# Optimization experiments

Measured on AMD Instinct MI355X. Metric: run time of the kernel, lower is better.

## Reference

```python
import jax, jax.numpy as jnp
import numpy as np

B, N, E = 8, 2000, 32000
LAT, STY, NF = 128, 64, 10
HEADS, HID = 4, 128
OUT = 3 + NF  # 13
EPS = 1e-5
SLOPE = 0.2


def _lin(k, fi, fo):
    return jax.random.normal(k, (fi, fo), dtype=jnp.float32) / np.sqrt(fi)


def setup_inputs() -> dict:
    key = jax.random.key(0)
    ks = jax.random.split(key, 32)
    inp = {
        'z': jax.random.normal(ks[0], (B, LAT), dtype=jnp.float32),
        'template_x': jax.random.normal(ks[1], (N, NF), dtype=jnp.float32),
        'template_edge_index': jax.random.randint(ks[2], (2, E), 0, N, dtype=jnp.int32),
        # style MLP
        'mlp_w1': _lin(ks[3], LAT, 256), 'mlp_b1': jnp.zeros((256,), jnp.float32),
        'mlp_w2': _lin(ks[4], 256, 512), 'mlp_b2': jnp.zeros((512,), jnp.float32),
        'mlp_w3': _lin(ks[5], 512, STY), 'mlp_b3': jnp.zeros((STY,), jnp.float32),
        # GAT1: in = NF + STY = 74 -> heads*HID = 512, concat
        'gat1_w': _lin(ks[6], NF + STY, HEADS * HID),
        'gat1_as': jax.random.normal(ks[7], (HEADS, HID), jnp.float32) * 0.1,
        'gat1_ad': jax.random.normal(ks[8], (HEADS, HID), jnp.float32) * 0.1,
        'gat1_b': jnp.zeros((HEADS * HID,), jnp.float32),
        'ln1_g': jnp.ones((HEADS * HID,), jnp.float32), 'ln1_b': jnp.zeros((HEADS * HID,), jnp.float32),
        # GAT2: 512 -> 512, concat
        'gat2_w': _lin(ks[9], HEADS * HID, HEADS * HID),
        'gat2_as': jax.random.normal(ks[10], (HEADS, HID), jnp.float32) * 0.1,
        'gat2_ad': jax.random.normal(ks[11], (HEADS, HID), jnp.float32) * 0.1,
        'gat2_b': jnp.zeros((HEADS * HID,), jnp.float32),
        'ln2_g': jnp.ones((HEADS * HID,), jnp.float32), 'ln2_b': jnp.zeros((HEADS * HID,), jnp.float32),
        # GAT3: 512 -> 13, 1 head, no concat
        'gat3_w': _lin(ks[12], HEADS * HID, OUT),
        'gat3_as': jax.random.normal(ks[13], (1, OUT), jnp.float32) * 0.1,
        'gat3_ad': jax.random.normal(ks[14], (1, OUT), jnp.float32) * 0.1,
        'gat3_b': jnp.zeros((OUT,), jnp.float32),
    }
    return inp


def gat_conv(x, src, dst, n_nodes, W, a_src, a_dst, bias, heads, out_ch, concat):
    # x: [NT, F_in]; per-head linear transform
    h = (x @ W).reshape(-1, heads, out_ch)              # [NT, H, C]
    als = jnp.sum(h * a_src[None], axis=-1)             # [NT, H]
    ald = jnp.sum(h * a_dst[None], axis=-1)             # [NT, H]
    logits = jax.nn.leaky_relu(als[src] + ald[dst], SLOPE)   # [E, H]
    # segment softmax over destination nodes (self-loops guarantee nonempty segments)
    mx = jax.ops.segment_max(logits, dst, num_segments=n_nodes)
    alpha = jnp.exp(logits - mx[dst])
    den = jax.ops.segment_sum(alpha, dst, num_segments=n_nodes)
    alpha = alpha / den[dst]                             # [E, H]
    msgs = h[src] * alpha[:, :, None]                    # [E, H, C]
    out = jax.ops.segment_sum(msgs, dst, num_segments=n_nodes)  # [NT, H, C]
    if concat:
        return out.reshape(n_nodes, heads * out_ch) + bias
    return out.mean(axis=1) + bias


def layer_norm(x, g, b):
    mu = jnp.mean(x, axis=-1, keepdims=True)
    var = jnp.mean((x - mu) ** 2, axis=-1, keepdims=True)
    return (x - mu) * jax.lax.rsqrt(var + EPS) * g + b


def reference(z, template_x, template_edge_index,
              mlp_w1, mlp_b1, mlp_w2, mlp_b2, mlp_w3, mlp_b3,
              gat1_w, gat1_as, gat1_ad, gat1_b, ln1_g, ln1_b,
              gat2_w, gat2_as, gat2_ad, gat2_b, ln2_g, ln2_b,
              gat3_w, gat3_as, gat3_ad, gat3_b):
    bsz = z.shape[0]
    n = template_x.shape[0]
    nt = bsz * n
    # batch the template graph: replicate nodes, offset edge indices per graph
    x = jnp.tile(template_x, (bsz, 1))                                  # [NT, NF]
    off = (jnp.arange(bsz, dtype=template_edge_index.dtype) * n)
    ei = (template_edge_index[:, None, :] + off[None, :, None]).reshape(2, -1)  # [2, B*E]
    loops = jnp.arange(nt, dtype=ei.dtype)
    src = jnp.concatenate([ei[0], loops])
    dst = jnp.concatenate([ei[1], loops])
    # style MLP
    s = jax.nn.leaky_relu(z @ mlp_w1 + mlp_b1, SLOPE)
    s = jax.nn.leaky_relu(s @ mlp_w2 + mlp_b2, SLOPE)
    s = s @ mlp_w3 + mlp_b3                                             # [B, STY]
    s_exp = jnp.repeat(s, n, axis=0)                                    # [NT, STY]
    H0 = jnp.concatenate([x, s_exp], axis=1)
    H1 = jax.nn.leaky_relu(gat_conv(H0, src, dst, nt, gat1_w, gat1_as, gat1_ad, gat1_b, HEADS, HID, True), SLOPE)
    H1n = layer_norm(H1, ln1_g, ln1_b)
    H2 = jax.nn.leaky_relu(gat_conv(H1n, src, dst, nt, gat2_w, gat2_as, gat2_ad, gat2_b, HEADS, HID, True), SLOPE)
    H2 = H2 + H1n
    H2n = layer_norm(H2, ln2_g, ln2_b)
    H_out = gat_conv(H2n, src, dst, nt, gat3_w, gat3_as, gat3_ad, gat3_b, 1, OUT, False)  # [NT, 13]
    delta_p = H_out[:, :3]
    delta_f = H_out[:, 3:]
    p_gen = x[:, :3] + delta_p
    X_gen = jnp.concatenate([p_gen, x[:, 3:] + delta_f[:, 3:]], axis=1)  # X[:, :3] overwritten by p_gen
    EF = p_gen[ei[1]] - p_gen[ei[0]]                                     # edge displacement vectors [B*E, 3]
    return X_gen, p_gen, EF
```

## Files before the change

### kernel.cpp

```cpp
#include <hip/hip_runtime.h>
#include <hip/hip_fp16.h>

constexpr int Bz = 8, Nn = 2000, Ee = 32000, NTOT = 16000;
constexpr int XG_OFF = 0, PG_OFF = 160000, EF_OFF = 208000;
#define SLOPE 0.2f
#define EPSL 1e-5f

typedef __attribute__((ext_vector_type(8))) _Float16 f16x8;
typedef __attribute__((ext_vector_type(4))) float float4v;

__device__ __forceinline__ float lrelu(float x) { return x > 0.f ? x : SLOPE * x; }

__device__ __forceinline__ unsigned short f2h(float x) {
  _Float16 hh = (_Float16)x;
  return *(unsigned short*)&hh;
}

__device__ __forceinline__ float wave_max(float v) {
  for (int o = 32; o; o >>= 1) v = fmaxf(v, __shfl_xor(v, o));
  return v;
}
__device__ __forceinline__ float wave_sum(float v) {
  for (int o = 32; o; o >>= 1) v += __shfl_xor(v, o);
  return v;
}

__global__ void hist_k(const int* __restrict__ tei, int* __restrict__ counts) {
  int j = blockIdx.x * 256 + threadIdx.x;
  if (j < Ee) atomicAdd(&counts[tei[Ee + j]], 1);
}

__global__ void scan_k(const int* __restrict__ counts, int* __restrict__ offs) {
  __shared__ int part[256];
  int t = threadIdx.x;
  int loc[8];
  int s = 0;
  for (int i = 0; i < 8; i++) {
    int idx = t * 8 + i;
    int c = (idx < Nn) ? counts[idx] : 0;
    loc[i] = s; s += c;
  }
  part[t] = s;
  __syncthreads();
  for (int o = 1; o < 256; o <<= 1) {
    int v = (t >= o) ? part[t - o] : 0;
    __syncthreads();
    part[t] += v;
    __syncthreads();
  }
  int excl = (t == 0) ? 0 : part[t - 1];
  for (int i = 0; i < 8; i++) {
    int idx = t * 8 + i;
    if (idx < Nn) offs[idx] = excl + loc[i];
  }
  if (t == 255) offs[Nn] = part[255];
}

__global__ void place_k(const int* __restrict__ tei, const int* __restrict__ offs,
                        int* __restrict__ cursor, int* __restrict__ colb) {
  int j = blockIdx.x * 256 + threadIdx.x;
  if (j < Ee) {
    int d = tei[Ee + j];
    int slot = offs[d] + atomicAdd(&cursor[d], 1);
    colb[slot] = tei[j];
  }
}

template <int K, int ACT>
__global__ __launch_bounds__(256) void lin_k(const float* __restrict__ x, const float* __restrict__ w,
                                             const float* __restrict__ bias, float* __restrict__ y,
                                             int O) {
  int gw = blockIdx.x * 4 + (threadIdx.x >> 6);
  int lane = threadIdx.x & 63;
  int bb = gw / O, o = gw - bb * O;
  float acc = 0.f;
#pragma unroll
  for (int k = lane; k < K; k += 64) acc += x[bb * K + k] * w[k * O + o];
  acc = wave_sum(acc);
  if (lane == 0) {
    if (bias) acc += bias[o];
    y[gw] = ACT ? lrelu(acc) : acc;
  }
}

__global__ __launch_bounds__(256) void w2bf_k(const float* __restrict__ W, unsigned short* __restrict__ Bt) {
  __shared__ float tile[32][33];
  int tx = threadIdx.x & 31, ty = threadIdx.x >> 5;
  int x0 = blockIdx.x * 32;
  int y0 = blockIdx.y * 32;
  for (int r = ty; r < 32; r += 8) tile[r][tx] = W[(y0 + r) * 512 + x0 + tx];
  __syncthreads();
  for (int r = ty; r < 32; r += 8) {
    unsigned short v = f2h(tile[tx][r]);
    size_t off = (size_t)(x0 + r) * 512 + (y0 + tx);
#pragma unroll
    for (int cp = 0; cp < 8; cp++) Bt[cp * 262144 + off] = v;
  }
}

__global__ void w3t_k(const float* __restrict__ W, unsigned short* __restrict__ W3t) {
  for (int idx = threadIdx.x; idx < 8192; idx += 256) {
    int col = idx >> 9, k = idx & 511;
    float v = (col < 13) ? W[k * 13 + col] : 0.f;
    W3t[idx] = f2h(v);
  }
}

__global__ __launch_bounds__(256) void wals_k(const float* __restrict__ g2w,
                                              const float* __restrict__ a_s, const float* __restrict__ a_d,
                                              float* __restrict__ wals, float* __restrict__ wald) {
  int c = blockIdx.x;
  int h = threadIdx.x >> 6, lane = threadIdx.x & 63;
  float sa = 0.f, sd = 0.f;
#pragma unroll
  for (int j = lane; j < 128; j += 64) {
    float wv = g2w[c * 512 + h * 128 + j];
    sa += wv * a_s[h * 128 + j];
    sd += wv * a_d[h * 128 + j];
  }
  sa = wave_sum(sa); sd = wave_sum(sd);
  if (lane == 0) { wals[c * 4 + h] = sa; wald[c * 4 + h] = sd; }
}

__global__ __launch_bounds__(256) void tp16_k(const float* __restrict__ tx, const float* __restrict__ g1w,
                                              const float* __restrict__ a_s, const float* __restrict__ a_d,
                                              unsigned short* __restrict__ tp16, float* __restrict__ tpa,
                                              float* __restrict__ tpd) {
  int nl = blockIdx.x;
  int head = threadIdx.x >> 6, lane = threadIdx.x & 63;
  int c = head * 128 + 2 * lane;
  float t0 = 0.f, t1 = 0.f;
#pragma unroll
  for (int k = 0; k < 10; k++) {
    float xv = tx[nl * 10 + k];
    float2 wv = *(const float2*)&g1w[k * 512 + c];
    t0 += xv * wv.x; t1 += xv * wv.y;
  }
  ushort2 st; st.x = f2h(t0); st.y = f2h(t1);
  *(ushort2*)&tp16[(size_t)nl * 512 + c] = st;
  float2 av = *(const float2*)&a_s[c];
  float2 dv = *(const float2*)&a_d[c];
  float pa = wave_sum(t0 * av.x + t1 * av.y);
  float pd = wave_sum(t0 * dv.x + t1 * dv.y);
  if (lane == 0) { tpa[nl * 4 + head] = pa; tpd[nl * 4 + head] = pd; }
}

__global__ void pba_k(const float* __restrict__ pb, const float* __restrict__ a_s,
                      const float* __restrict__ a_d, float* __restrict__ pba, float* __restrict__ pbd) {
  int b = blockIdx.x >> 2, h = blockIdx.x & 3;
  int lane = threadIdx.x;
  int c = h * 128 + 2 * lane;
  float2 pv = *(const float2*)&pb[b * 512 + c];
  float2 av = *(const float2*)&a_s[c];
  float2 dv = *(const float2*)&a_d[c];
  float pa = wave_sum(pv.x * av.x + pv.y * av.y);
  float pd = wave_sum(pv.x * dv.x + pv.y * dv.y);
  if (lane == 0) { pba[b * 4 + h] = pa; pbd[b * 4 + h] = pd; }
}

__global__ __launch_bounds__(256) void agg1_k(const unsigned short* __restrict__ tp16,
                                              const float* __restrict__ tpa, const float* __restrict__ tpd,
                                              const float* __restrict__ pba, const float* __restrict__ pbd,
                                              const float* __restrict__ pb,
                                              const float* __restrict__ bias,
                                              const float* __restrict__ g, const float* __restrict__ beta,
                                              const float* __restrict__ wals, const float* __restrict__ wald,
                                              unsigned short* __restrict__ out,
                                              float* __restrict__ als2, float* __restrict__ ald2,
                                              const int* __restrict__ offs, const int* __restrict__ colb) {
  int blk = blockIdx.x;
  int b = blk & 7, nl = blk >> 3;
  int n = b * Nn + nl;
  int w = threadIdx.x >> 6, lane = threadIdx.x & 63;
  int rs = offs[nl];
  int nit = offs[nl + 1] - rs + 1;
  float aldn = tpd[nl * 4 + w] + pbd[b * 4 + w];
  float pbsrc = pba[b * 4 + w];

  __shared__ unsigned int alpha_u[4][68];
  __shared__ int sgn[64];
  __shared__ float part[4][512];
  __shared__ float invs[4];
  __shared__ float red[8];
  __shared__ float red2[4][8];
  __shared__ float bcs[2];

  __half2 acc2[4];
#pragma unroll
  for (int j = 0; j < 4; j++) acc2[j] = __float2half2_rn(0.f);

  const unsigned short* hbase = tp16 + lane * 8;
  int hd = lane >> 4;

  if (nit <= 64) {
    int se = nl;
    float logit = -3e38f;
    if (lane < nit) {
      se = (lane < nit - 1) ? colb[rs + lane] : nl;
      logit = lrelu(tpa[se * 4 + w] + pbsrc + aldn);
    }
    if (w == 0) sgn[lane] = se;
    float m = wave_max(logit);
    float raw = (lane < nit) ? __expf(logit - m) : 0.f;
    float den = wave_sum(raw);
    if (lane == 0) invs[w] = 1.f / den;
    __half2 a2 = __float2half2_rn(raw);
    alpha_u[w][lane] = *(unsigned int*)&a2;
    __syncthreads();
    int e = w;
    for (; e + 12 < nit; e += 16) {
      uint4 hv[4];
      unsigned int au[4];
#pragma unroll
      for (int i = 0; i < 4; i++) {
        int ei = e + i * 4;
        au[i] = alpha_u[hd][ei];
        hv[i] = *(const uint4*)(hbase + (size_t)sgn[ei] * 512);
      }
#pragma unroll
      for (int i = 0; i < 4; i++) {
        __half2 a2e = *(__half2*)&au[i];
        acc2[0] = __hfma2(a2e, *(__half2*)&hv[i].x, acc2[0]);
        acc2[1] = __hfma2(a2e, *(__half2*)&hv[i].y, acc2[1]);
        acc2[2] = __hfma2(a2e, *(__half2*)&hv[i].z, acc2[2]);
        acc2[3] = __hfma2(a2e, *(__half2*)&hv[i].w, acc2[3]);
      }
    }
    for (; e < nit; e += 4) {
      unsigned int au = alpha_u[hd][e];
      uint4 hv = *(const uint4*)(hbase + (size_t)sgn[e] * 512);
      __half2 a2e = *(__half2*)&au;
      acc2[0] = __hfma2(a2e, *(__half2*)&hv.x, acc2[0]);
      acc2[1] = __hfma2(a2e, *(__half2*)&hv.y, acc2[1]);
      acc2[2] = __hfma2(a2e, *(__half2*)&hv.z, acc2[2]);
      acc2[3] = __hfma2(a2e, *(__half2*)&hv.w, acc2[3]);
    }
  } else {
    float m = -3e38f;
    for (int i = lane; i < nit; i += 64) {
      int se = (i < nit - 1) ? colb[rs + i] : nl;
      m = fmaxf(m, lrelu(tpa[se * 4 + w] + pbsrc + aldn));
    }
    m = wave_max(m);
    float den = 0.f;
    for (int base = 0; base < nit; base += 64) {
      int cnt = min(64, nit - base);
      int se = nl;
      float raw = 0.f;
      if (lane < cnt) {
        int i = base + lane;
        se = (i < nit - 1) ? colb[rs + i] : nl;
        raw = __expf(lrelu(tpa[se * 4 + w] + pbsrc + aldn) - m);
      }
      if (w == 0) sgn[lane] = se;
      den += raw;
      __half2 a2 = __float2half2_rn(raw);
      alpha_u[w][lane] = *(unsigned int*)&a2;
      __syncthreads();
      for (int e = w; e < cnt; e += 4) {
        unsigned int au = alpha_u[hd][e];
        uint4 hv = *(const uint4*)(hbase + (size_t)sgn[e] * 512);
        __half2 a2e = *(__half2*)&au;
        acc2[0] = __hfma2(a2e, *(__half2*)&hv.x, acc2[0]);
        acc2[1] = __hfma2(a2e, *(__half2*)&hv.y, acc2[1]);
        acc2[2] = __hfma2(a2e, *(__half2*)&hv.z, acc2[2]);
        acc2[3] = __hfma2(a2e, *(__half2*)&hv.w, acc2[3]);
      }
      __syncthreads();
    }
    den = wave_sum(den);
    if (lane == 0) invs[w] = 1.f / den;
  }

  float fv[8];
#pragma unroll
  for (int j = 0; j < 4; j++) {
    float2 f2 = __half22float2(acc2[j]);
    fv[2 * j] = f2.x; fv[2 * j + 1] = f2.y;
  }
  *(float4*)&part[w][lane * 8] = make_float4(fv[0], fv[1], fv[2], fv[3]);
  *(float4*)&part[w][lane * 8 + 4] = make_float4(fv[4], fv[5], fv[6], fv[7]);
  __syncthreads();

  int c = 2 * (int)threadIdx.x;
  float inv = invs[c >> 7];
  float s0 = part[0][c] + part[1][c] + part[2][c] + part[3][c];
  float s1 = part[0][c + 1] + part[1][c + 1] + part[2][c + 1] + part[3][c + 1];
  float2 pv = *(const float2*)&pb[b * 512 + c];
  float v0 = lrelu(s0 * inv + pv.x + bias[c]);
  float v1 = lrelu(s1 * inv + pv.y + bias[c + 1]);
  float p1 = wave_sum(v0 + v1);
  float p2 = wave_sum(v0 * v0 + v1 * v1);
  if (lane == 0) { red[w] = p1; red[4 + w] = p2; }
  __syncthreads();
  if (threadIdx.x == 0) {
    float s1r = red[0] + red[1] + red[2] + red[3];
    float s2r = red[4] + red[5] + red[6] + red[7];
    float mu = s1r * (1.f / 512.f);
    float var = s2r * (1.f / 512.f) - mu * mu;
    bcs[0] = mu;
    bcs[1] = rsqrtf(var + EPSL);
  }
  __syncthreads();
  float mu = bcs[0], rstd = bcs[1];
  float o0 = (v0 - mu) * rstd * g[c] + beta[c];
  float o1 = (v1 - mu) * rstd * g[c + 1] + beta[c + 1];
  ushort2 st; st.x = f2h(o0); st.y = f2h(o1);
  *(ushort2*)&out[(size_t)n * 512 + c] = st;

  float4 wa0 = *(const float4*)&wals[c * 4];
  float4 wa1 = *(const float4*)&wals[(c + 1) * 4];
  float4 wd0 = *(const float4*)&wald[c * 4];
  float4 wd1 = *(const float4*)&wald[(c + 1) * 4];
  float sv[8];
  sv[0] = o0 * wa0.x + o1 * wa1.x; sv[1] = o0 * wa0.y + o1 * wa1.y;
  sv[2] = o0 * wa0.z + o1 * wa1.z; sv[3] = o0 * wa0.w + o1 * wa1.w;
  sv[4] = o0 * wd0.x + o1 * wd1.x; sv[5] = o0 * wd0.y + o1 * wd1.y;
  sv[6] = o0 * wd0.z + o1 * wd1.z; sv[7] = o0 * wd0.w + o1 * wd1.w;
#pragma unroll
  for (int j = 0; j < 8; j++) sv[j] = wave_sum(sv[j]);
  if (lane == 0) {
#pragma unroll
    for (int j = 0; j < 8; j++) red2[w][j] = sv[j];
  }
  __syncthreads();
  if (threadIdx.x < 8) {
    int j = threadIdx.x;
    float v = red2[0][j] + red2[1][j] + red2[2][j] + red2[3][j];
    if (j < 4) als2[n * 4 + j] = v;
    else ald2[n * 4 + (j - 4)] = v;
  }
}

__global__ __launch_bounds__(256) void agg_k(const unsigned short* __restrict__ h,
                                             const float* __restrict__ als, const float* __restrict__ ald,
                                             const float* __restrict__ bias,
                                             const float* __restrict__ g, const float* __restrict__ beta,
                                             const unsigned short* __restrict__ resid,
                                             unsigned short* __restrict__ out,
                                             const int* __restrict__ offs, const int* __restrict__ colb) {
  int blk = blockIdx.x;
  int b = blk & 7, nl = blk >> 3;
  int n = b * Nn + nl;
  int w = threadIdx.x >> 6, lane = threadIdx.x & 63;
  int rs = offs[nl];
  int nit = offs[nl + 1] - rs + 1;
  float aldn = ald[n * 4 + w];

  __shared__ unsigned int alpha_u[4][68];
  __shared__ int sgn[64];
  __shared__ float part[4][512];
  __shared__ float invs[4];
  __shared__ float red[8];
  __shared__ float bcs[2];

  __half2 acc2[4];
#pragma unroll
  for (int j = 0; j < 4; j++) acc2[j] = __float2half2_rn(0.f);

  const unsigned short* hbase = h + lane * 8;
  int hd = lane >> 4;

  if (nit <= 64) {
    int sg = n;
    float logit = -3e38f;
    if (lane < nit) {
      sg = (lane < nit - 1) ? colb[rs + lane] + b * Nn : n;
      logit = lrelu(als[sg * 4 + w] + aldn);
    }
    if (w == 0) sgn[lane] = sg;
    float m = wave_max(logit);
    float raw = (lane < nit) ? __expf(logit - m) : 0.f;
    float den = wave_sum(raw);
    if (lane == 0) invs[w] = 1.f / den;
    __half2 a2 = __float2half2_rn(raw);
    alpha_u[w][lane] = *(unsigned int*)&a2;
    __syncthreads();
    int e = w;
    for (; e + 12 < nit; e += 16) {
      uint4 hv[4];
      unsigned int au[4];
#pragma unroll
      for (int i = 0; i < 4; i++) {
        int ei = e + i * 4;
        au[i] = alpha_u[hd][ei];
        hv[i] = *(const uint4*)(hbase + (size_t)sgn[ei] * 512);
      }
#pragma unroll
      for (int i = 0; i < 4; i++) {
        __half2 a2e = *(__half2*)&au[i];
        acc2[0] = __hfma2(a2e, *(__half2*)&hv[i].x, acc2[0]);
        acc2[1] = __hfma2(a2e, *(__half2*)&hv[i].y, acc2[1]);
        acc2[2] = __hfma2(a2e, *(__half2*)&hv[i].z, acc2[2]);
        acc2[3] = __hfma2(a2e, *(__half2*)&hv[i].w, acc2[3]);
      }
    }
    for (; e < nit; e += 4) {
      unsigned int au = alpha_u[hd][e];
      uint4 hv = *(const uint4*)(hbase + (size_t)sgn[e] * 512);
      __half2 a2e = *(__half2*)&au;
      acc2[0] = __hfma2(a2e, *(__half2*)&hv.x, acc2[0]);
      acc2[1] = __hfma2(a2e, *(__half2*)&hv.y, acc2[1]);
      acc2[2] = __hfma2(a2e, *(__half2*)&hv.z, acc2[2]);
      acc2[3] = __hfma2(a2e, *(__half2*)&hv.w, acc2[3]);
    }
  } else {
    float m = -3e38f;
    for (int i = lane; i < nit; i += 64) {
      int sg = (i < nit - 1) ? colb[rs + i] + b * Nn : n;
      m = fmaxf(m, lrelu(als[sg * 4 + w] + aldn));
    }
    m = wave_max(m);
    float den = 0.f;
    for (int base = 0; base < nit; base += 64) {
      int cnt = min(64, nit - base);
      int sg = n;
      float raw = 0.f;
      if (lane < cnt) {
        int i = base + lane;
        sg = (i < nit - 1) ? colb[rs + i] + b * Nn : n;
        raw = __expf(lrelu(als[sg * 4 + w] + aldn) - m);
      }
      if (w == 0) sgn[lane] = sg;
      den += raw;
      __half2 a2 = __float2half2_rn(raw);
      alpha_u[w][lane] = *(unsigned int*)&a2;
      __syncthreads();
      for (int e = w; e < cnt; e += 4) {
        unsigned int au = alpha_u[hd][e];
        uint4 hv = *(const uint4*)(hbase + (size_t)sgn[e] * 512);
        __half2 a2e = *(__half2*)&au;
        acc2[0] = __hfma2(a2e, *(__half2*)&hv.x, acc2[0]);
        acc2[1] = __hfma2(a2e, *(__half2*)&hv.y, acc2[1]);
        acc2[2] = __hfma2(a2e, *(__half2*)&hv.z, acc2[2]);
        acc2[3] = __hfma2(a2e, *(__half2*)&hv.w, acc2[3]);
      }
      __syncthreads();
    }
    den = wave_sum(den);
    if (lane == 0) invs[w] = 1.f / den;
  }

  float fv[8];
#pragma unroll
  for (int j = 0; j < 4; j++) {
    float2 f2 = __half22float2(acc2[j]);
    fv[2 * j] = f2.x; fv[2 * j + 1] = f2.y;
  }
  *(float4*)&part[w][lane * 8] = make_float4(fv[0], fv[1], fv[2], fv[3]);
  *(float4*)&part[w][lane * 8 + 4] = make_float4(fv[4], fv[5], fv[6], fv[7]);
  __syncthreads();

  int c = 2 * (int)threadIdx.x;
  float inv = invs[c >> 7];
  float s0 = part[0][c] + part[1][c] + part[2][c] + part[3][c];
  float s1 = part[0][c + 1] + part[1][c + 1] + part[2][c + 1] + part[3][c + 1];
  float v0 = lrelu(s0 * inv + bias[c]);
  float v1 = lrelu(s1 * inv + bias[c + 1]);
  unsigned int rv = *(const unsigned int*)&resid[(size_t)n * 512 + c];
  __half2 rh = *(__half2*)&rv;
  float2 rf = __half22float2(rh);
  v0 += rf.x; v1 += rf.y;
  float p1 = wave_sum(v0 + v1);
  float p2 = wave_sum(v0 * v0 + v1 * v1);
  if (lane == 0) { red[w] = p1; red[4 + w] = p2; }
  __syncthreads();
  if (threadIdx.x == 0) {
    float s1r = red[0] + red[1] + red[2] + red[3];
    float s2r = red[4] + red[5] + red[6] + red[7];
    float mu = s1r * (1.f / 512.f);
    float var = s2r * (1.f / 512.f) - mu * mu;
    bcs[0] = mu;
    bcs[1] = rsqrtf(var + EPSL);
  }
  __syncthreads();
  float mu = bcs[0], rstd = bcs[1];
  float o0 = (v0 - mu) * rstd * g[c] + beta[c];
  float o1 = (v1 - mu) * rstd * g[c + 1] + beta[c + 1];
  ushort2 st; st.x = f2h(o0); st.y = f2h(o1);
  *(ushort2*)&out[(size_t)n * 512 + c] = st;
}

__global__ __launch_bounds__(256) void gemm2_k(const unsigned short* __restrict__ A,
                                               const unsigned short* __restrict__ Bt,
                                               unsigned short* __restrict__ C) {
  __shared__ unsigned short sB[64][520];
  int t = threadIdx.x;
  int lane = t & 63, w = t >> 6;
  int m0 = blockIdx.x * 128;
  int n0 = blockIdx.y * 64;
  const unsigned short* Bl = Bt + (size_t)((blockIdx.x + blockIdx.y * 125) & 7) * 262144;

#pragma unroll
  for (int q = 0; q < 16; q++) {
    int slot = q * 256 + t;
    int row = slot >> 6, c16 = (slot & 63) * 8;
    *(uint4*)&sB[row][c16] = *(const uint4*)(Bl + (size_t)(n0 + row) * 512 + c16);
  }
  __syncthreads();

  float4v acc[2][4];
#pragma unroll
  for (int m = 0; m < 2; m++)
#pragma unroll
    for (int nn = 0; nn < 4; nn++) acc[m][nn] = (float4v){0.f, 0.f, 0.f, 0.f};

  int r0 = m0 + w * 32 + (lane & 15);
  int kb = (lane >> 4) * 8;
  const unsigned short* a0p = A + (size_t)r0 * 512 + kb;
  const unsigned short* a1p = A + (size_t)(r0 + 16) * 512 + kb;
  int bc = lane & 15;

#pragma unroll
  for (int kf = 0; kf < 16; kf++) {
    int k0 = kf * 32;
    f16x8 af0 = *(const f16x8*)(a0p + k0);
    f16x8 af1 = *(const f16x8*)(a1p + k0);
    f16x8 bg0 = *(const f16x8*)&sB[bc][k0 + kb];
    f16x8 bg1 = *(const f16x8*)&sB[16 + bc][k0 + kb];
    f16x8 bg2 = *(const f16x8*)&sB[32 + bc][k0 + kb];
    f16x8 bg3 = *(const f16x8*)&sB[48 + bc][k0 + kb];
    acc[0][0] = __builtin_amdgcn_mfma_f32_16x16x32_f16(af0, bg0, acc[0][0], 0, 0, 0);
    acc[0][1] = __builtin_amdgcn_mfma_f32_16x16x32_f16(af0, bg1, acc[0][1], 0, 0, 0);
    acc[0][2] = __builtin_amdgcn_mfma_f32_16x16x32_f16(af0, bg2, acc[0][2], 0, 0, 0);
    acc[0][3] = __builtin_amdgcn_mfma_f32_16x16x32_f16(af0, bg3, acc[0][3], 0, 0, 0);
    acc[1][0] = __builtin_amdgcn_mfma_f32_16x16x32_f16(af1, bg0, acc[1][0], 0, 0, 0);
    acc[1][1] = __builtin_amdgcn_mfma_f32_16x16x32_f16(af1, bg1, acc[1][1], 0, 0, 0);
    acc[1][2] = __builtin_amdgcn_mfma_f32_16x16x32_f16(af1, bg2, acc[1][2], 0, 0, 0);
    acc[1][3] = __builtin_amdgcn_mfma_f32_16x16x32_f16(af1, bg3, acc[1][3], 0, 0, 0);
  }

  __syncthreads();
  unsigned short* sC = &sB[0][0];
  int rb = w * 32 + (lane >> 4) * 4;
#pragma unroll
  for (int m = 0; m < 2; m++)
#pragma unroll
    for (int nn = 0; nn < 4; nn++)
#pragma unroll
      for (int r = 0; r < 4; r++)
        sC[(rb + m * 16 + r) * 72 + bc + nn * 16] = f2h(acc[m][nn][r]);
  __syncthreads();
#pragma unroll
  for (int p = 0; p < 4; p++) {
    int row = p * 32 + (t >> 3);
    int co = (t & 7) * 8;
    uint4 v = *(const uint4*)&sC[row * 72 + co];
    *(uint4*)&C[(size_t)(m0 + row) * 512 + n0 + co] = v;
  }
}

__global__ __launch_bounds__(256) void gemm3_k(const unsigned short* __restrict__ H,
                                               const unsigned short* __restrict__ W3t,
                                               const float* __restrict__ as3, const float* __restrict__ ad3,
                                               float* __restrict__ h3, float* __restrict__ als3,
                                               float* __restrict__ ald3) {
  int w = threadIdx.x >> 6, l = threadIdx.x & 63;
  int blk = blockIdx.x;
  int b = blk & 7, i = blk >> 3;
  int base = i * 64 + w * 16;
  int r16 = l & 15, g4 = l >> 4;
  int lrow_ld = min(base + r16, Nn - 1);
  float4v acc = (float4v){0.f, 0.f, 0.f, 0.f};
  const unsigned short* ha = H + (size_t)(b * Nn + lrow_ld) * 512 + g4 * 8;
  const unsigned short* wb = W3t + (size_t)r16 * 512 + g4 * 8;
#pragma unroll
  for (int kk = 0; kk < 16; kk++) {
    f16x8 a = *(const f16x8*)(ha + kk * 32);
    f16x8 bfr = *(const f16x8*)(wb + kk * 32);
    acc = __builtin_amdgcn_mfma_f32_16x16x32_f16(a, bfr, acc, 0, 0, 0);
  }
  int col = r16;
  float asv = (col < 13) ? as3[col] : 0.f;
  float adv = (col < 13) ? ad3[col] : 0.f;
#pragma unroll
  for (int r = 0; r < 4; r++) {
    float v = acc[r];
    int lrow = base + g4 * 4 + r;
    if (lrow < Nn) {
      int row = b * Nn + lrow;
      if (col < 13) h3[row * 13 + col] = v;
      float sa = v * asv, sd = v * adv;
      for (int o = 1; o < 16; o <<= 1) { sa += __shfl_xor(sa, o); sd += __shfl_xor(sd, o); }
      if (col == 0) { als3[row] = sa; ald3[row] = sd; }
    }
  }
}

__global__ __launch_bounds__(64) void agg3_k(const float* __restrict__ h3, const float* __restrict__ als3,
                                             const float* __restrict__ ald3, const float* __restrict__ b3,
                                             const float* __restrict__ tx, const int* __restrict__ offs,
                                             const int* __restrict__ colb, float* __restrict__ dout) {
  int blk = blockIdx.x, lane = threadIdx.x;
  int b = blk & 7, nl = blk >> 3;
  int n = b * Nn + nl;
  int rs = offs[nl], deg = offs[nl + 1] - rs;
  float aldn = ald3[n];
  float sl = lrelu(als3[n] + aldn);
  float a = 0.f, inv;
  if (deg <= 64) {
    int sgl = 0; float logit = -1e30f;
    if (lane < deg) { sgl = colb[rs + lane] + b * Nn; logit = lrelu(als3[sgl] + aldn); }
    float m = wave_max(fmaxf(logit, sl));
    float raw = (lane < deg) ? __expf(logit - m) : 0.f;
    float es = __expf(sl - m);
    inv = 1.f / (wave_sum(raw) + es);
    if (lane < 13) a = es * h3[n * 13 + lane];
    for (int e = 0; e < deg; e++) {
      float w = __shfl(raw, e);
      int sg = __shfl(sgl, e);
      if (lane < 13) a += w * h3[sg * 13 + lane];
    }
  } else {
    float m = sl;
    for (int e = lane; e < deg; e += 64) {
      int sg = colb[rs + e] + b * Nn;
      m = fmaxf(m, lrelu(als3[sg] + aldn));
    }
    m = wave_max(m);
    float es = __expf(sl - m);
    float den = (lane == 0) ? es : 0.f;
    if (lane < 13) a = es * h3[n * 13 + lane];
    for (int base = 0; base < deg; base += 64) {
      int cnt = min(64, deg - base);
      int sgl = 0; float raw = 0.f;
      if (lane < cnt) {
        sgl = colb[rs + base + lane] + b * Nn;
        raw = __expf(lrelu(als3[sgl] + aldn) - m);
      }
      den += raw;
      for (int e = 0; e < cnt; e++) {
        float w = __shfl(raw, e);
        int sg = __shfl(sgl, e);
        if (lane < 13) a += w * h3[sg * 13 + lane];
      }
    }
    inv = 1.f / wave_sum(den);
  }
  a *= inv;
  float hv = a + ((lane < 13) ? b3[lane] : 0.f);
  float txv = (lane < 10) ? tx[nl * 10 + lane] : 0.f;
  float pv = txv + hv;
  if (lane < 3) dout[PG_OFF + n * 3 + lane] = pv;
  float up = __shfl(hv, lane + 3);
  float xg = (lane < 3) ? pv : (txv + up);
  if (lane < 10) dout[XG_OFF + n * 10 + lane] = xg;
}

__global__ void ef_k(const int* __restrict__ tei, float* __restrict__ dout) {
  int blk = blockIdx.x;
  int b = blk & 7, i = blk >> 3;
  int j = i * 256 + threadIdx.x;
  int e = b * Ee + j;
  int sg = tei[j] + b * Nn;
  int dg = tei[Ee + j] + b * Nn;
  const float* pg = dout + PG_OFF;
  dout[EF_OFF + e * 3 + 0] = pg[dg * 3 + 0] - pg[sg * 3 + 0];
  dout[EF_OFF + e * 3 + 1] = pg[dg * 3 + 1] - pg[sg * 3 + 1];
  dout[EF_OFF + e * 3 + 2] = pg[dg * 3 + 2] - pg[sg * 3 + 2];
}

extern "C" void kernel_launch(void* const* d_in, const int* in_sizes, int n_in,
                              void* d_out, int out_size, void* d_ws, size_t ws_size,
                              hipStream_t stream) {
  const float* z = (const float*)d_in[0];
  const float* tx = (const float*)d_in[1];
  const int* tei = (const int*)d_in[2];
  const float* w1 = (const float*)d_in[3];
  const float* b1 = (const float*)d_in[4];
  const float* w2 = (const float*)d_in[5];
  const float* b2 = (const float*)d_in[6];
  const float* w3 = (const float*)d_in[7];
  const float* b3 = (const float*)d_in[8];
  const float* g1w = (const float*)d_in[9];
  const float* g1as = (const float*)d_in[10];
  const float* g1ad = (const float*)d_in[11];
  const float* g1b = (const float*)d_in[12];
  const float* ln1g = (const float*)d_in[13];
  const float* ln1b = (const float*)d_in[14];
  const float* g2w = (const float*)d_in[15];
  const float* g2as = (const float*)d_in[16];
  const float* g2ad = (const float*)d_in[17];
  const float* g2b = (const float*)d_in[18];
  const float* ln2g = (const float*)d_in[19];
  const float* ln2b = (const float*)d_in[20];
  const float* g3w = (const float*)d_in[21];
  const float* g3as = (const float*)d_in[22];
  const float* g3ad = (const float*)d_in[23];
  const float* g3b = (const float*)d_in[24];
  float* out = (float*)d_out;

  float* F = (float*)d_ws;
  float* pb_ = F + 0;
  float* l1_ = F + 8192;
  float* l2_ = F + 16384;
  float* s_ = F + 24576;
  float* pba_ = F + 30000;
  float* pbd_ = F + 30100;
  float* wals_ = F + 40000;
  float* wald_ = F + 50000;
  float* tpa_ = F + 100000;
  float* tpd_ = F + 164000;
  float* als2 = F + 228000;
  float* ald2 = F + 292000;
  float* als3 = F + 356000;
  float* ald3 = F + 372000;
  float* h3_ = F + 388000;
  unsigned short* U = (unsigned short*)(F + 600000);
  unsigned short* hA = U;
  unsigned short* hB = U + 8192000;
  unsigned short* Bt = U + 16384000;
  unsigned short* W3t = U + 18481152;
  unsigned short* tp16 = U + 18489344;
  int* I = (int*)(F + 12000000);
  int* counts = I;
  int* cursor = I + 2000;
  int* offs = I + 4000;
  int* colb = I + 6001;

  hipMemsetAsync(counts, 0, 4000 * sizeof(int), stream);
  hist_k<<<125, 256, 0, stream>>>(tei, counts);
  scan_k<<<1, 256, 0, stream>>>(counts, offs);
  place_k<<<125, 256, 0, stream>>>(tei, offs, cursor, colb);

  w2bf_k<<<dim3(16, 16), 256, 0, stream>>>(g2w, Bt);
  w3t_k<<<1, 256, 0, stream>>>(g3w, W3t);
  wals_k<<<512, 256, 0, stream>>>(g2w, g2as, g2ad, wals_, wald_);
  tp16_k<<<Nn, 256, 0, stream>>>(tx, g1w, g1as, g1ad, tp16, tpa_, tpd_);

  lin_k<128, 1><<<512, 256, 0, stream>>>(z, w1, b1, l1_, 256);
  lin_k<256, 1><<<1024, 256, 0, stream>>>(l1_, w2, b2, l2_, 512);
  lin_k<512, 0><<<128, 256, 0, stream>>>(l2_, w3, b3, s_, 64);
  lin_k<64, 0><<<1024, 256, 0, stream>>>(s_, g1w + 10 * 512, nullptr, pb_, 512);
  pba_k<<<32, 64, 0, stream>>>(pb_, g1as, g1ad, pba_, pbd_);

  agg1_k<<<NTOT, 256, 0, stream>>>(tp16, tpa_, tpd_, pba_, pbd_, pb_, g1b, ln1g, ln1b,
                                   wals_, wald_, hB, als2, ald2, offs, colb);

  gemm2_k<<<dim3(125, 8), 256, 0, stream>>>(hB, Bt, hA);
  agg_k<<<NTOT, 256, 0, stream>>>(hA, als2, ald2, g2b, ln2g, ln2b, hB, hB, offs, colb);

  gemm3_k<<<256, 256, 0, stream>>>(hB, W3t, g3as, g3ad, h3_, als3, ald3);
  agg3_k<<<NTOT, 64, 0, stream>>>(h3_, als3, ald3, g3b, tx, offs, colb, out);
  ef_k<<<1000, 256, 0, stream>>>(tei, out);
}
```

Before: 211.2 us.

## Compute GAT2 attention logits in gemm2 epilogue instead of agg1 precomputed weights

Removes the wals_k kernel and the per-node attention-score projection from agg1_k, which used precomputed W·a vectors and an extra block-wide reduction and barrier. Instead, gemm2_k reduces its accumulator tile against a_src/a_dst in the epilogue and atomically adds partial sums into als2/ald2. Two memsets zero those buffers first. This trades a kernel launch and agg1 reduction work for float atomics across the 8 column blocks, which makes the summation order nondeterministic.

```diff
diff --git a/kernel.cpp b/kernel.cpp
--- a/kernel.cpp
+++ b/kernel.cpp
@@ -104,22 +104,6 @@
     float v = (col < 13) ? W[k * 13 + col] : 0.f;
     W3t[idx] = f2h(v);
   }
-}
-
-__global__ __launch_bounds__(256) void wals_k(const float* __restrict__ g2w,
-                                              const float* __restrict__ a_s, const float* __restrict__ a_d,
-                                              float* __restrict__ wals, float* __restrict__ wald) {
-  int c = blockIdx.x;
-  int h = threadIdx.x >> 6, lane = threadIdx.x & 63;
-  float sa = 0.f, sd = 0.f;
-#pragma unroll
-  for (int j = lane; j < 128; j += 64) {
-    float wv = g2w[c * 512 + h * 128 + j];
-    sa += wv * a_s[h * 128 + j];
-    sd += wv * a_d[h * 128 + j];
-  }
-  sa = wave_sum(sa); sd = wave_sum(sd);
-  if (lane == 0) { wals[c * 4 + h] = sa; wald[c * 4 + h] = sd; }
 }
 
 __global__ __launch_bounds__(256) void tp16_k(const float* __restrict__ tx, const float* __restrict__ g1w,
@@ -164,9 +148,7 @@
                                               const float* __restrict__ pb,
                                               const float* __restrict__ bias,
                                               const float* __restrict__ g, const float* __restrict__ beta,
-                                              const float* __restrict__ wals, const float* __restrict__ wald,
                                               unsigned short* __restrict__ out,
-                                              float* __restrict__ als2, float* __restrict__ ald2,
                                               const int* __restrict__ offs, const int* __restrict__ colb) {
   int blk = blockIdx.x;
   int b = blk & 7, nl = blk >> 3;
@@ -182,7 +164,6 @@
   __shared__ float part[4][512];
   __shared__ float invs[4];
   __shared__ float red[8];
-  __shared__ float red2[4][8];
   __shared__ float bcs[2];
 
   __half2 acc2[4];
@@ -307,29 +288,6 @@
   float o1 = (v1 - mu) * rstd * g[c + 1] + beta[c + 1];
   ushort2 st; st.x = f2h(o0); st.y = f2h(o1);
   *(ushort2*)&out[(size_t)n * 512 + c] = st;
-
-  float4 wa0 = *(const float4*)&wals[c * 4];
-  float4 wa1 = *(const float4*)&wals[(c + 1) * 4];
-  float4 wd0 = *(const float4*)&wald[c * 4];
-  float4 wd1 = *(const float4*)&wald[(c + 1) * 4];
-  float sv[8];
-  sv[0] = o0 * wa0.x + o1 * wa1.x; sv[1] = o0 * wa0.y + o1 * wa1.y;
-  sv[2] = o0 * wa0.z + o1 * wa1.z; sv[3] = o0 * wa0.w + o1 * wa1.w;
-  sv[4] = o0 * wd0.x + o1 * wd1.x; sv[5] = o0 * wd0.y + o1 * wd1.y;
-  sv[6] = o0 * wd0.z + o1 * wd1.z; sv[7] = o0 * wd0.w + o1 * wd1.w;
-#pragma unroll
-  for (int j = 0; j < 8; j++) sv[j] = wave_sum(sv[j]);
-  if (lane == 0) {
-#pragma unroll
-    for (int j = 0; j < 8; j++) red2[w][j] = sv[j];
-  }
-  __syncthreads();
-  if (threadIdx.x < 8) {
-    int j = threadIdx.x;
-    float v = red2[0][j] + red2[1][j] + red2[2][j] + red2[3][j];
-    if (j < 4) als2[n * 4 + j] = v;
-    else ald2[n * 4 + (j - 4)] = v;
-  }
 }
 
 __global__ __launch_bounds__(256) void agg_k(const unsigned short* __restrict__ h,
@@ -483,7 +441,9 @@
 
 __global__ __launch_bounds__(256) void gemm2_k(const unsigned short* __restrict__ A,
                                                const unsigned short* __restrict__ Bt,
-                                               unsigned short* __restrict__ C) {
+                                               unsigned short* __restrict__ C,
+                                               const float* __restrict__ As, const float* __restrict__ Ad,
+                                               float* __restrict__ als2, float* __restrict__ ald2) {
   __shared__ unsigned short sB[64][520];
   int t = threadIdx.x;
   int lane = t & 63, w = t >> 6;
@@ -528,6 +488,32 @@
     acc[1][1] = __builtin_amdgcn_mfma_f32_16x16x32_f16(af1, bg1, acc[1][1], 0, 0, 0);
     acc[1][2] = __builtin_amdgcn_mfma_f32_16x16x32_f16(af1, bg2, acc[1][2], 0, 0, 0);
     acc[1][3] = __builtin_amdgcn_mfma_f32_16x16x32_f16(af1, bg3, acc[1][3], 0, 0, 0);
+  }
+
+  {
+    int head = n0 >> 7;
+    int cb = n0 & 127;
+    float asv[4], adv[4];
+#pragma unroll
+    for (int nn = 0; nn < 4; nn++) {
+      asv[nn] = As[head * 128 + cb + nn * 16 + bc];
+      adv[nn] = Ad[head * 128 + cb + nn * 16 + bc];
+    }
+#pragma unroll
+    for (int m = 0; m < 2; m++) {
+#pragma unroll
+      for (int r = 0; r < 4; r++) {
+        float pa = 0.f, pd = 0.f;
+#pragma unroll
+        for (int nn = 0; nn < 4; nn++) { pa += acc[m][nn][r] * asv[nn]; pd += acc[m][nn][r] * adv[nn]; }
+        for (int o = 1; o < 16; o <<= 1) { pa += __shfl_xor(pa, o); pd += __shfl_xor(pd, o); }
+        if ((lane & 15) == 0) {
+          int row = m0 + w * 32 + (lane >> 4) * 4 + m * 16 + r;
+          atomicAdd(&als2[row * 4 + head], pa);
+          atomicAdd(&ald2[row * 4 + head], pd);
+        }
+      }
+    }
   }
 
   __syncthreads();
@@ -697,8 +683,6 @@
   float* s_ = F + 24576;
   float* pba_ = F + 30000;
   float* pbd_ = F + 30100;
-  float* wals_ = F + 40000;
-  float* wald_ = F + 50000;
   float* tpa_ = F + 100000;
   float* tpd_ = F + 164000;
   float* als2 = F + 228000;
@@ -719,13 +703,15 @@
   int* colb = I + 6001;
 
   hipMemsetAsync(counts, 0, 4000 * sizeof(int), stream);
+  hipMemsetAsync(als2, 0, 64000 * sizeof(float), stream);
+  hipMemsetAsync(ald2, 0, 64000 * sizeof(float), stream);
+
   hist_k<<<125, 256, 0, stream>>>(tei, counts);
   scan_k<<<1, 256, 0, stream>>>(counts, offs);
   place_k<<<125, 256, 0, stream>>>(tei, offs, cursor, colb);
 
   w2bf_k<<<dim3(16, 16), 256, 0, stream>>>(g2w, Bt);
   w3t_k<<<1, 256, 0, stream>>>(g3w, W3t);
-  wals_k<<<512, 256, 0, stream>>>(g2w, g2as, g2ad, wals_, wald_);
   tp16_k<<<Nn, 256, 0, stream>>>(tx, g1w, g1as, g1ad, tp16, tpa_, tpd_);
 
   lin_k<128, 1><<<512, 256, 0, stream>>>(z, w1, b1, l1_, 256);
@@ -735,9 +721,9 @@
   pba_k<<<32, 64, 0, stream>>>(pb_, g1as, g1ad, pba_, pbd_);
 
   agg1_k<<<NTOT, 256, 0, stream>>>(tp16, tpa_, tpd_, pba_, pbd_, pb_, g1b, ln1g, ln1b,
-                                   wals_, wald_, hB, als2, ald2, offs, colb);
-
-  gemm2_k<<<dim3(125, 8), 256, 0, stream>>>(hB, Bt, hA);
+                                   hB, offs, colb);
+
+  gemm2_k<<<dim3(125, 8), 256, 0, stream>>>(hB, Bt, hA, g2as, g2ad, als2, ald2);
   agg_k<<<NTOT, 256, 0, stream>>>(hA, als2, ald2, g2b, ln2g, ln2b, hB, hB, offs, colb);
 
   gemm3_k<<<256, 256, 0, stream>>>(hB, W3t, g3as, g3ad, h3_, als3, ald3);
```

After: 193.7 us. -8.3%, faster.
